# Optimization experiments

Hardware: AMD Instinct MI355X
Metric: run time of the kernel (lower is better)

Reference implementation:

```python
import jax, jax.numpy as jnp
import numpy as np
from jax import lax

# dims: B batch, L seq len, D channels, N SSM state size
BATCH, L, D, N = 8, 2048, 256, 64
MIN_DELTA = 1e-6
EPS = 1e-6


def setup_inputs() -> dict:
    key = jax.random.key(0)
    k0, k1, k2, k3, k4 = jax.random.split(key, 5)
    x = jax.random.normal(k0, (BATCH, L, D), dtype=jnp.float32)
    # log_A chosen so A = softplus(log_A) is small -> discrete_A^L stays finite in fp32
    log_A = -jax.random.normal(k1, (N, N), dtype=jnp.float32) - 3.0
    Bp = jax.random.normal(k2, (D, N), dtype=jnp.float32) * 0.02
    Cp = jax.random.normal(k3, (D, N), dtype=jnp.float32) * 0.02
    log_delta = jnp.full((D,), -8.0, dtype=jnp.float32)  # dt ~ 3.4e-4 (stability)
    skip_D = jnp.ones((D,), dtype=jnp.float32)
    W_out = jax.random.normal(k4, (D, D), dtype=jnp.float32) * (1.0 / np.sqrt(D))
    b_out = jnp.zeros((D,), dtype=jnp.float32)
    return dict(x=x, log_A=log_A, Bp=Bp, Cp=Cp, log_delta=log_delta,
                skip_D=skip_D, W_out=W_out, b_out=b_out)


def reference(x, log_A, Bp, Cp, log_delta, skip_D, W_out, b_out):
    Bsz, Lx, Dx = x.shape
    # --- discretize ---
    A = jax.nn.softplus(log_A)                                  # [N,N]
    dt = jax.nn.softplus(log_delta) + MIN_DELTA                 # [D]
    dA = jax.vmap(jax.scipy.linalg.expm)(A[None] * dt[:, None, None])  # [D,N,N]
    I = jnp.eye(A.shape[0], dtype=A.dtype)
    X = jnp.linalg.solve(A + EPS * I, Bp.T)                     # [N,D] = A^{-1} B^T
    dB = jnp.einsum('dnm,dm->dn', dA - I, X.T)                  # [D,N]
    # --- kernel k[d,l] = C_d . (dA_d)^l dB_d, via sequential recurrence (same math
    # as the explicit A-power loop, carrying the vector instead of the matrix) ---
    def step(v, _):
        return jnp.einsum('dnm,dm->dn', dA, v), jnp.sum(Cp * v, axis=-1)
    _, ks = lax.scan(step, dB, None, length=Lx)                 # ks: [L,D]
    k = ks.T                                                    # [D,L]
    # --- grouped causal conv1d: y[b,d,t] = sum_tau k[d,tau] x[b,d,t-tau] ---
    w = jnp.flip(k, -1)[:, None, :]                             # [D,1,L]
    y = lax.conv_general_dilated(
        jnp.transpose(x, (0, 2, 1)), w, (1,), [(Lx - 1, 0)],
        dimension_numbers=('NCH', 'OIH', 'NCH'), feature_group_count=Dx)
    y = jnp.transpose(y, (0, 2, 1))                             # [B,L,D]
    return (y + x * skip_D) @ W_out.T + b_out
```

## Files before the change

kernel.cpp:

```cpp
#include <hip/hip_runtime.h>

#define Bz 8
#define Lz 2048
#define Dz 256
#define Nz 64
#define SP 68
#define SA 65
#define SM 132
#define SAK 40
#define KE 4
#define KP 7
#define BSP 4
#define BPB (Bz / BSP)

typedef __attribute__((ext_vector_type(8))) short bf16x8;
typedef __attribute__((ext_vector_type(4))) float f32x4;

__device__ __forceinline__ float softplusf(float x) {
  return (x > 20.f) ? x : log1pf(expf(x));
}

__device__ __forceinline__ unsigned short f2bf(float f) {
  unsigned int u = __float_as_uint(f);
  u += 0x7fffu + ((u >> 16) & 1u);
  return (unsigned short)(u >> 16);
}

__device__ __forceinline__ void pmm_acc(const float* __restrict__ LA,
                                        const float* __restrict__ LB,
                                        float* acc, int n, int q) {
  float arow[64];
#pragma unroll
  for (int mm = 0; mm < 16; ++mm) {
    const float4 a4 = *(const float4*)(LA + n * SP + mm * 4);
    arow[4 * mm + 0] = a4.x; arow[4 * mm + 1] = a4.y;
    arow[4 * mm + 2] = a4.z; arow[4 * mm + 3] = a4.w;
  }
#pragma unroll
  for (int i = 0; i < 16; ++i) acc[i] = 0.f;
#pragma unroll 8
  for (int m = 0; m < 64; ++m) {
    const float4 b0 = *(const float4*)(LB + m * SP + q * 16 + 0);
    const float4 b1 = *(const float4*)(LB + m * SP + q * 16 + 4);
    const float4 b2 = *(const float4*)(LB + m * SP + q * 16 + 8);
    const float4 b3 = *(const float4*)(LB + m * SP + q * 16 + 12);
    const float a = arow[m];
    acc[0]  = fmaf(a, b0.x, acc[0]);  acc[1]  = fmaf(a, b0.y, acc[1]);
    acc[2]  = fmaf(a, b0.z, acc[2]);  acc[3]  = fmaf(a, b0.w, acc[3]);
    acc[4]  = fmaf(a, b1.x, acc[4]);  acc[5]  = fmaf(a, b1.y, acc[5]);
    acc[6]  = fmaf(a, b1.z, acc[6]);  acc[7]  = fmaf(a, b1.w, acc[7]);
    acc[8]  = fmaf(a, b2.x, acc[8]);  acc[9]  = fmaf(a, b2.y, acc[9]);
    acc[10] = fmaf(a, b2.z, acc[10]); acc[11] = fmaf(a, b2.w, acc[11]);
    acc[12] = fmaf(a, b3.x, acc[12]); acc[13] = fmaf(a, b3.y, acc[13]);
    acc[14] = fmaf(a, b3.z, acc[14]); acc[15] = fmaf(a, b3.w, acc[15]);
  }
}

__global__ __launch_bounds__(256) void s4_xt(const float* __restrict__ x,
                                             float* __restrict__ xT,
                                             const float* __restrict__ log_A,
                                             float* __restrict__ Apow) {
  if (blockIdx.x == 0 && blockIdx.y == 0) {
    const int i = blockIdx.z * 512 + threadIdx.x;
    Apow[i] = softplusf(log_A[i]);
    Apow[i + 256] = softplusf(log_A[i + 256]);
  }
  __shared__ float tile[64][69];
  const int t0 = blockIdx.x * 64, d0 = blockIdx.y * 64, b = blockIdx.z;
  const int rr = threadIdx.x >> 4;
  const int c4 = (threadIdx.x & 15) * 4;
#pragma unroll
  for (int p = 0; p < 4; ++p) {
    const int row = p * 16 + rr;
    const float4 v = *(const float4*)(x + ((size_t)b * Lz + t0 + row) * Dz + d0 + c4);
    tile[row][c4 + 0] = v.x; tile[row][c4 + 1] = v.y;
    tile[row][c4 + 2] = v.z; tile[row][c4 + 3] = v.w;
  }
  __syncthreads();
#pragma unroll
  for (int p = 0; p < 4; ++p) {
    const int dd = p * 16 + rr;
    float4 o;
    o.x = tile[c4 + 0][dd]; o.y = tile[c4 + 1][dd];
    o.z = tile[c4 + 2][dd]; o.w = tile[c4 + 3][dd];
    *(float4*)(xT + ((size_t)(d0 + dd) * Bz + b) * Lz + t0 + c4) = o;
  }
}

__global__ __launch_bounds__(256, 1) void s4_buildpow(
    float* __restrict__ Apow, const float* __restrict__ Bp,
    const float* __restrict__ Cp, const float* __restrict__ log_delta,
    float* __restrict__ Gk, float* __restrict__ Qk,
    float* __restrict__ kloc, float* __restrict__ dts) {
  __shared__ float As[Nz * SA];
  __shared__ float Pst[KP + 1][Nz];
  __shared__ float Qst[KE + 1][Nz];
  __shared__ float Pv[Nz], Qv[Nz], dBs[Nz];
  __shared__ float prA[4][Nz + 8], prB[4][Nz + 8];
  __shared__ float zp[KE + 1][17], zs[KE + 1];
  __shared__ alignas(16) float PA[Nz * SP];
  __shared__ alignas(16) float PB[Nz * SP];
  const int tid = threadIdx.x;
  const int d = blockIdx.x;
  const int n = tid & 63, qq = tid >> 6;

  if (d >= Dz) {
    const int role = d - Dz;
#pragma unroll
    for (int i = 0; i < 4; ++i) {
      const int e = (tid + 256 * i) * 4;
      const int r = e >> 6, c = e & 63;
      const float4 v = *(const float4*)(Apow + e);
      *(float4*)&PA[r * SP + c] = v;
      *(float4*)&PB[r * SP + c] = v;
    }
    __syncthreads();
    float acc[16];
    pmm_acc(PA, PB, acc, n, qq);
    if (role == 0) {
      float* O = Apow + (size_t)1 * 4096;
#pragma unroll
      for (int v = 0; v < 4; ++v) {
        float4 o;
        o.x = acc[4 * v]; o.y = acc[4 * v + 1];
        o.z = acc[4 * v + 2]; o.w = acc[4 * v + 3];
        *(float4*)(O + n * 64 + qq * 16 + 4 * v) = o;
      }
      return;
    }
    __syncthreads();
#pragma unroll
    for (int i = 0; i < 16; ++i) {
      PB[n * SP + qq * 16 + i] = acc[i];
      if (role == 2) PA[n * SP + qq * 16 + i] = acc[i];
    }
    __syncthreads();
    pmm_acc(PA, PB, acc, n, qq);
    float* O = Apow + (size_t)(role + 1) * 4096;
#pragma unroll
    for (int v = 0; v < 4; ++v) {
      float4 o;
      o.x = acc[4 * v]; o.y = acc[4 * v + 1];
      o.z = acc[4 * v + 2]; o.w = acc[4 * v + 3];
      *(float4*)(O + n * 64 + qq * 16 + 4 * v) = o;
    }
    return;
  }

  const float dt = softplusf(log_delta[d]) + 1e-6f;
#pragma unroll
  for (int i = 0; i < 4; ++i) {
    const int e = (tid + 256 * i) * 4;
    const int r = e >> 6, c = e & 63;
    const float4 v = *(const float4*)(Apow + e);
    As[r * SA + c] = v.x; As[r * SA + c + 1] = v.y;
    As[r * SA + c + 2] = v.z; As[r * SA + c + 3] = v.w;
  }
  if (tid < 64) {
    const float bv = Bp[d * Nz + tid], cv = Cp[d * Nz + tid];
    Pv[tid] = bv; Pst[0][tid] = bv;
    Qv[tid] = cv; Qst[0][tid] = cv;
  }
  __syncthreads();
#pragma unroll 1
  for (int k = 1; k <= KP; ++k) {
    float pp = 0.f, pq = 0.f;
#pragma unroll
    for (int mm = 0; mm < 16; ++mm) {
      const int m = qq * 16 + mm;
      pp += As[n * SA + m] * Pv[m];
      pq += As[m * SA + n] * Qv[m];
    }
    prA[qq][n] = pp; prB[qq][n] = pq;
    __syncthreads();
    if (tid < 64) {
      const float np = prA[0][tid] + prA[1][tid] + prA[2][tid] + prA[3][tid];
      Pv[tid] = np; Pst[k][tid] = np;
      if (k <= KE) {
        const float nq = prB[0][tid] + prB[1][tid] + prB[2][tid] + prB[3][tid];
        Qv[tid] = nq; Qst[k][tid] = nq;
      }
    }
    __syncthreads();
  }
  const float dtc0 = dt;
  const float dtc1 = dt * dt * 0.5f;
  const float dtc2 = dtc1 * dt * (1.f / 3.f);
  const float dtc3 = dtc2 * dt * 0.25f;
  if (tid < 64) {
    dBs[tid] = dtc0 * Pst[0][tid] + dtc1 * Pst[1][tid] +
               dtc2 * Pst[2][tid] + dtc3 * Pst[3][tid];
#pragma unroll
    for (int k = 0; k <= KE; ++k) {
      Gk[(size_t)d * ((KE + 1) * 64) + k * 64 + tid] =
          dtc0 * Pst[k][tid] + dtc1 * Pst[k + 1][tid] +
          dtc2 * Pst[k + 2][tid] + dtc3 * Pst[k + 3][tid];
      Qk[(size_t)d * ((KE + 1) * 64) + k * 64 + tid] = Qst[k][tid];
    }
  }
  __syncthreads();
  if (tid < (KE + 1) * 16) {
    const int k = tid >> 4, seg = tid & 15;
    float s = 0.f;
#pragma unroll
    for (int i = 0; i < 4; ++i) s += Qst[k][seg * 4 + i] * dBs[seg * 4 + i];
    zp[k][seg] = s;
  }
  __syncthreads();
  if (tid <= KE) {
    float s = 0.f;
#pragma unroll
    for (int seg = 0; seg < 16; ++seg) s += zp[tid][seg];
    zs[tid] = s;
  }
  __syncthreads();
  if (tid < 64) {
    const float rdt = (float)tid * dt;
    float c = 1.f, acc = zs[0];
#pragma unroll
    for (int k = 1; k <= KE; ++k) { c *= rdt / (float)k; acc += c * zs[k]; }
    kloc[d * 64 + tid] = acc;
  }
  if (tid == 0) dts[d] = dt;
}

__global__ __launch_bounds__(256) void s4_scan4(
    const float* __restrict__ xT, const float* __restrict__ Apow,
    const float* __restrict__ Gk, const float* __restrict__ dts,
    float* __restrict__ S) {
  __shared__ float Es[Nz * SA];
  __shared__ float Gs[(KE + 1) * Nz];
  __shared__ float CTs[KE + 1][66];
  __shared__ alignas(16) float Xs[BPB][64];
  __shared__ alignas(16) float Ss[BPB][64];
  __shared__ float pr[4][BPB][64];
  const int d = blockIdx.x;
  const int z = blockIdx.y;
  const int tid = threadIdx.x, n = tid & 63, q = tid >> 6;
  const int rb = tid >> 6;
  const float dt = dts[d];
  if (tid < 65) {
    const float rdt = (float)tid * dt;
    float c = 1.f;
    CTs[0][tid] = 1.f;
#pragma unroll
    for (int k = 1; k <= KE; ++k) { c *= rdt / (float)k; CTs[k][tid] = c; }
  }
  for (int idx = tid; idx < (KE + 1) * 64; idx += 256)
    Gs[idx] = Gk[(size_t)d * ((KE + 1) * 64) + idx];
  {
    float ea[16];
#pragma unroll
    for (int i = 0; i < 16; ++i) ea[i] = 0.f;
    const float dt64 = 64.f * dt;
    float ce = 1.f;
#pragma unroll 1
    for (int k = 1; k <= KE; ++k) {
      ce *= dt64 / (float)k;
      const float* Ak = Apow + (size_t)(k - 1) * 4096;
#pragma unroll
      for (int i = 0; i < 16; ++i)
        ea[i] = fmaf(ce, Ak[tid + 256 * i], ea[i]);
    }
#pragma unroll
    for (int i = 0; i < 16; ++i) {
      const int e = tid + 256 * i;
      const int r = e >> 6, c = e & 63;
      Es[r * SA + c] = ea[i] + ((r == c) ? 1.f : 0.f);
    }
  }
  __syncthreads();
  float Er[16], Ur[16];
#pragma unroll
  for (int i = 0; i < 16; ++i) Er[i] = Es[n * SA + q * 16 + i];
#pragma unroll
  for (int i = 0; i < 16; ++i) {
    const int j = q * 16 + i;
    float u = 0.f;
#pragma unroll
    for (int k = 0; k <= KE; ++k) u = fmaf(CTs[k][63 - j], Gs[k * 64 + n], u);
    Ur[i] = u;
  }
  if (rb < BPB) Ss[rb][n] = 0.f;
  const float* xd = xT + ((size_t)d * Bz + z * BPB) * Lz;
  float* Sd = S + (size_t)d * (32 * 8 * 64) + (size_t)(z * BPB) * 64;
#pragma unroll 1
  for (int c = 0; c < 32; ++c) {
    if (rb < BPB) {
      Xs[rb][n] = xd[(size_t)rb * Lz + c * 64 + n];
      Sd[c * 512 + rb * 64 + n] = Ss[rb][n];
    }
    __syncthreads();
    float acc[BPB];
#pragma unroll
    for (int b = 0; b < BPB; ++b) {
      const float4 s0 = *(const float4*)&Ss[b][q * 16 + 0];
      const float4 s1 = *(const float4*)&Ss[b][q * 16 + 4];
      const float4 s2 = *(const float4*)&Ss[b][q * 16 + 8];
      const float4 s3 = *(const float4*)&Ss[b][q * 16 + 12];
      const float4 x0 = *(const float4*)&Xs[b][q * 16 + 0];
      const float4 x1 = *(const float4*)&Xs[b][q * 16 + 4];
      const float4 x2 = *(const float4*)&Xs[b][q * 16 + 8];
      const float4 x3 = *(const float4*)&Xs[b][q * 16 + 12];
      float a = 0.f;
      a = fmaf(Er[0], s0.x, a);  a = fmaf(Er[1], s0.y, a);
      a = fmaf(Er[2], s0.z, a);  a = fmaf(Er[3], s0.w, a);
      a = fmaf(Er[4], s1.x, a);  a = fmaf(Er[5], s1.y, a);
      a = fmaf(Er[6], s1.z, a);  a = fmaf(Er[7], s1.w, a);
      a = fmaf(Er[8], s2.x, a);  a = fmaf(Er[9], s2.y, a);
      a = fmaf(Er[10], s2.z, a); a = fmaf(Er[11], s2.w, a);
      a = fmaf(Er[12], s3.x, a); a = fmaf(Er[13], s3.y, a);
      a = fmaf(Er[14], s3.z, a); a = fmaf(Er[15], s3.w, a);
      a = fmaf(Ur[0], x0.x, a);  a = fmaf(Ur[1], x0.y, a);
      a = fmaf(Ur[2], x0.z, a);  a = fmaf(Ur[3], x0.w, a);
      a = fmaf(Ur[4], x1.x, a);  a = fmaf(Ur[5], x1.y, a);
      a = fmaf(Ur[6], x1.z, a);  a = fmaf(Ur[7], x1.w, a);
      a = fmaf(Ur[8], x2.x, a);  a = fmaf(Ur[9], x2.y, a);
      a = fmaf(Ur[10], x2.z, a); a = fmaf(Ur[11], x2.w, a);
      a = fmaf(Ur[12], x3.x, a); a = fmaf(Ur[13], x3.y, a);
      a = fmaf(Ur[14], x3.z, a); a = fmaf(Ur[15], x3.w, a);
      acc[b] = a;
    }
#pragma unroll
    for (int b = 0; b < BPB; ++b) pr[q][b][n] = acc[b];
    __syncthreads();
    if (rb < BPB)
      Ss[rb][n] = pr[0][rb][n] + pr[1][rb][n] + pr[2][rb][n] + pr[3][rb][n];
    __syncthreads();
  }
}

__global__ __launch_bounds__(256, 2) void s4_out6(
    const float* __restrict__ xT, const float* __restrict__ S,
    const float* __restrict__ Qk, const float* __restrict__ kloc,
    const float* __restrict__ dts, const float* __restrict__ skip_D,
    unsigned short* __restrict__ yb) {
  __shared__ alignas(16) float Ms[64 * SM];
  __shared__ alignas(16) float Zs[64 * SM];
  __shared__ float Qs[(KE + 1) * Nz];
  __shared__ float CT[KE + 1][66];
  __shared__ float kx[64];
  const int d = blockIdx.x;
  const int ch = blockIdx.y;
  const int tid = threadIdx.x;
  const int tc = tid & 15, tr = tid >> 4;
  const float dt = dts[d];
  const float sd = skip_D[d];
  if (tid < 65) {
    const float rdt = (float)tid * dt;
    float c = 1.f;
    CT[0][tid] = 1.f;
#pragma unroll
    for (int k = 1; k <= KE; ++k) { c *= rdt / (float)k; CT[k][tid] = c; }
  }
  for (int idx = tid; idx < (KE + 1) * 64; idx += 256)
    Qs[idx] = Qk[(size_t)d * ((KE + 1) * 64) + idx];
  if (tid < 64) kx[tid] = kloc[d * 64 + tid];
  __syncthreads();
#pragma unroll
  for (int i = 0; i < 16; ++i) {
    const int e = tid + 256 * i;
    const int r = e >> 6, m = e & 63;
    float w = 0.f;
#pragma unroll
    for (int k = 0; k <= KE; ++k) w = fmaf(CT[k][r + 1], Qs[k * 64 + m], w);
    Ms[r * SM + m] = w;
  }
#pragma unroll
  for (int i = 0; i < 16; ++i) {
    const int e = tid + 256 * i;
    const int r = e >> 6, j = e & 63;
    Ms[r * SM + 64 + j] = (j <= r) ? kx[r - j] : 0.f;
  }
  const float* xd = xT + (size_t)d * Bz * Lz;
  const float* Sd = S + (size_t)d * (32 * 8 * 64);
  const int lcol = tid >> 2, seg = tid & 3;
  const int sbb = lcol & 7, sccl = lcol >> 3;
  {
    const int cc = ch * 8 + sccl;
    const float* sp = Sd + cc * 512 + sbb * 64 + seg * 16;
    const float* xp = xd + (size_t)sbb * Lz + cc * 64 + seg * 16;
    float* zrow = Zs + lcol * SM;
#pragma unroll
    for (int i = 0; i < 4; ++i) {
      *(float4*)(zrow + seg * 16 + i * 4) = *(const float4*)(sp + i * 4);
      *(float4*)(zrow + 64 + seg * 16 + i * 4) = *(const float4*)(xp + i * 4);
    }
  }
  __syncthreads();
  float acc[16];
#pragma unroll
  for (int i = 0; i < 16; ++i) acc[i] = 0.f;
#pragma unroll 4
  for (int k = 0; k < 128; k += 4) {
    float4 mv[4], zv[4];
#pragma unroll
    for (int i = 0; i < 4; ++i)
      mv[i] = *(const float4*)&Ms[(tr * 4 + i) * SM + k];
#pragma unroll
    for (int jj = 0; jj < 4; ++jj)
      zv[jj] = *(const float4*)&Zs[(tc + 16 * jj) * SM + k];
#pragma unroll
    for (int i = 0; i < 4; ++i)
#pragma unroll
      for (int jj = 0; jj < 4; ++jj) {
        acc[i * 4 + jj] = fmaf(mv[i].x, zv[jj].x, acc[i * 4 + jj]);
        acc[i * 4 + jj] = fmaf(mv[i].y, zv[jj].y, acc[i * 4 + jj]);
        acc[i * 4 + jj] = fmaf(mv[i].z, zv[jj].z, acc[i * 4 + jj]);
        acc[i * 4 + jj] = fmaf(mv[i].w, zv[jj].w, acc[i * 4 + jj]);
      }
  }
#pragma unroll
  for (int i = 0; i < 4; ++i)
#pragma unroll
    for (int jj = 0; jj < 4; ++jj)
      acc[i * 4 + jj] =
          fmaf(sd, Zs[(tc + 16 * jj) * SM + 64 + tr * 4 + i], acc[i * 4 + jj]);
  __syncthreads();
#pragma unroll
  for (int i = 0; i < 4; ++i)
#pragma unroll
    for (int jj = 0; jj < 4; ++jj)
      Zs[(tc + 16 * jj) * SM + tr * 4 + i] = acc[i * 4 + jj];
  __syncthreads();
  {
    const int cc = ch * 8 + sccl;
    unsigned short* yp =
        yb + ((size_t)d * Bz + sbb) * Lz + cc * 64 + seg * 16;
    const float* zrow = Zs + lcol * SM;
#pragma unroll
    for (int i = 0; i < 4; ++i) {
      ushort4 o;
      o.x = f2bf(zrow[seg * 16 + i * 4 + 0]);
      o.y = f2bf(zrow[seg * 16 + i * 4 + 1]);
      o.z = f2bf(zrow[seg * 16 + i * 4 + 2]);
      o.w = f2bf(zrow[seg * 16 + i * 4 + 3]);
      *(ushort4*)(yp + i * 4) = o;
    }
  }
}

__global__ __launch_bounds__(256, 2) void s4_gemm4(
    const unsigned short* __restrict__ yb, const float* __restrict__ Wo,
    const float* __restrict__ bo, float* __restrict__ out) {
  __shared__ alignas(16) unsigned short LA[128 * SAK];
  __shared__ alignas(16) unsigned short LB[64 * SAK];
  const int tid = threadIdx.x;
  const int wave = tid >> 6, lane = tid & 63;
  const int quad = lane >> 4, lq = lane & 15;
  const int r0 = blockIdx.x * 128;
  const int c0 = blockIdx.y * 64;
  const int brow = r0 >> 11, t0 = r0 & 2047;
  const int ad = tid & 31;
  const int atp = tid >> 5;
  const int bc = tid >> 2;
  const int bko = tid & 3;
  f32x4 acc[2][4];
#pragma unroll
  for (int mi = 0; mi < 2; ++mi)
#pragma unroll
    for (int ni = 0; ni < 4; ++ni)
#pragma unroll
      for (int i = 0; i < 4; ++i) acc[mi][ni][i] = 0.f;
#pragma unroll 1
  for (int ks = 0; ks < 8; ++ks) {
    const int k0 = ks * 32;
    {
      const unsigned short* src =
          yb + ((size_t)(k0 + ad) * Bz + brow) * Lz + t0 + atp * 16;
#pragma unroll
      for (int h = 0; h < 2; ++h) {
        const bf16x8 v = *(const bf16x8*)(src + h * 8);
#pragma unroll
        for (int j = 0; j < 8; ++j)
          LA[(atp * 16 + h * 8 + j) * SAK + ad] = (unsigned short)v[j];
      }
    }
    {
      const float* wsrc = Wo + (size_t)(c0 + bc) * Dz + k0 + bko * 8;
      const float4 w0 = *(const float4*)(wsrc);
      const float4 w1 = *(const float4*)(wsrc + 4);
      bf16x8 wv;
      wv[0] = (short)f2bf(w0.x); wv[1] = (short)f2bf(w0.y);
      wv[2] = (short)f2bf(w0.z); wv[3] = (short)f2bf(w0.w);
      wv[4] = (short)f2bf(w1.x); wv[5] = (short)f2bf(w1.y);
      wv[6] = (short)f2bf(w1.z); wv[7] = (short)f2bf(w1.w);
      *(bf16x8*)&LB[bc * SAK + bko * 8] = wv;
    }
    __syncthreads();
    bf16x8 af[2], bfr[4];
#pragma unroll
    for (int mi = 0; mi < 2; ++mi)
      af[mi] = *(const bf16x8*)&LA[(wave * 32 + mi * 16 + lq) * SAK + quad * 8];
#pragma unroll
    for (int ni = 0; ni < 4; ++ni)
      bfr[ni] = *(const bf16x8*)&LB[(ni * 16 + lq) * SAK + quad * 8];
#pragma unroll
    for (int mi = 0; mi < 2; ++mi)
#pragma unroll
      for (int ni = 0; ni < 4; ++ni)
        acc[mi][ni] = __builtin_amdgcn_mfma_f32_16x16x32_bf16(
            af[mi], bfr[ni], acc[mi][ni], 0, 0, 0);
    __syncthreads();
  }
  float bb[4];
#pragma unroll
  for (int ni = 0; ni < 4; ++ni) bb[ni] = bo[c0 + ni * 16 + lq];
#pragma unroll
  for (int mi = 0; mi < 2; ++mi)
#pragma unroll
    for (int i = 0; i < 4; ++i) {
      const int row = r0 + wave * 32 + mi * 16 + quad * 4 + i;
#pragma unroll
      for (int ni = 0; ni < 4; ++ni)
        out[(size_t)row * Dz + c0 + ni * 16 + lq] = acc[mi][ni][i] + bb[ni];
    }
}

extern "C" void kernel_launch(void* const* d_in, const int* in_sizes, int n_in,
                              void* d_out, int out_size, void* d_ws, size_t ws_size,
                              hipStream_t stream) {
  const float* x         = (const float*)d_in[0];
  const float* log_A     = (const float*)d_in[1];
  const float* Bp        = (const float*)d_in[2];
  const float* Cp        = (const float*)d_in[3];
  const float* log_delta = (const float*)d_in[4];
  const float* skip_D    = (const float*)d_in[5];
  const float* W_out     = (const float*)d_in[6];
  const float* b_out     = (const float*)d_in[7];
  float* out = (float*)d_out;

  float* xT   = (float*)d_ws;
  float* ybf  = xT + (size_t)Dz * Bz * Lz;
  float* S    = ybf + (size_t)Dz * Bz * Lz;
  float* Apow = S + (size_t)Dz * (32 * 8 * 64);
  float* Gk   = Apow + (size_t)8 * 4096;
  float* Qk   = Gk + (size_t)Dz * (KE + 1) * 64;
  float* kloc = Qk + (size_t)Dz * (KE + 1) * 64;
  float* dts  = kloc + (size_t)Dz * 64;
  unsigned short* yb = (unsigned short*)ybf;

  hipLaunchKernelGGL(s4_xt, dim3(Lz / 64, Dz / 64, Bz), dim3(256), 0, stream,
                     x, xT, log_A, Apow);
  hipLaunchKernelGGL(s4_buildpow, dim3(Dz + 3), dim3(256), 0, stream,
                     Apow, Bp, Cp, log_delta, Gk, Qk, kloc, dts);
  hipLaunchKernelGGL(s4_scan4, dim3(Dz, BSP), dim3(256), 0, stream,
                     xT, Apow, Gk, dts, S);
  hipLaunchKernelGGL(s4_out6, dim3(Dz, 4), dim3(256), 0, stream,
                     xT, S, Qk, kloc, dts, skip_D, yb);
  hipLaunchKernelGGL(s4_gemm4, dim3((Bz * Lz) / 128, Dz / 64), dim3(256), 0, stream,
                     yb, W_out, b_out, out);
}
```

Before: 168.2 us.

## Convert output-chunk GEMM in s4_out to bf16 MFMA with folded skip term

Rewrites the per-channel output kernel so the 64x128 by 128x64 product runs on bf16 MFMA 16x16x32 instructions instead of scalar fp32 FMAs. Operands are converted to bf16 when staged into shared memory, which halves LDS footprint and allows more blocks per CU. The skip connection is folded into the local kernel diagonal, and results are written straight from accumulators without a shared-memory transpose. This trades precision, since state, inputs and kernel weights are now rounded to bf16, for much higher matrix throughput.

```diff
diff --git a/kernel.cpp b/kernel.cpp
--- a/kernel.cpp
+++ b/kernel.cpp
@@ -6,8 +6,8 @@
 #define Nz 64
 #define SP 68
 #define SA 65
-#define SM 132
 #define SAK 40
+#define SKB 136
 #define KE 4
 #define KP 7
 #define BSP 4
@@ -330,22 +330,22 @@
   }
 }
 
-__global__ __launch_bounds__(256, 2) void s4_out6(
+__global__ __launch_bounds__(256, 4) void s4_out7(
     const float* __restrict__ xT, const float* __restrict__ S,
     const float* __restrict__ Qk, const float* __restrict__ kloc,
     const float* __restrict__ dts, const float* __restrict__ skip_D,
     unsigned short* __restrict__ yb) {
-  __shared__ alignas(16) float Ms[64 * SM];
-  __shared__ alignas(16) float Zs[64 * SM];
+  __shared__ alignas(16) unsigned short Msb[64 * SKB];
+  __shared__ alignas(16) unsigned short Zsb[64 * SKB];
   __shared__ float Qs[(KE + 1) * Nz];
   __shared__ float CT[KE + 1][66];
-  __shared__ float kx[64];
+  __shared__ unsigned short kxb[64];
   const int d = blockIdx.x;
   const int ch = blockIdx.y;
   const int tid = threadIdx.x;
-  const int tc = tid & 15, tr = tid >> 4;
+  const int wave = tid >> 6, lane = tid & 63;
+  const int quad = lane >> 4, lq = lane & 15;
   const float dt = dts[d];
-  const float sd = skip_D[d];
   if (tid < 65) {
     const float rdt = (float)tid * dt;
     float c = 1.f;
@@ -355,8 +355,29 @@
   }
   for (int idx = tid; idx < (KE + 1) * 64; idx += 256)
     Qs[idx] = Qk[(size_t)d * ((KE + 1) * 64) + idx];
-  if (tid < 64) kx[tid] = kloc[d * 64 + tid];
-  __syncthreads();
+  if (tid < 64)
+    kxb[tid] = f2bf(kloc[d * 64 + tid] + ((tid == 0) ? skip_D[d] : 0.f));
+
+  const float* xd = xT + (size_t)d * Bz * Lz;
+  const float* Sd = S + (size_t)d * (32 * 8 * 64);
+#pragma unroll
+  for (int p = 0; p < 8; ++p) {
+    const int u = tid + 256 * p;
+    const int col = u >> 5;
+    const int sub = u & 31;
+    const int k0 = sub * 4;
+    const int bb = col & 7, ccl = col >> 3;
+    const int cc = ch * 8 + ccl;
+    const float* src = (k0 < 64)
+        ? (Sd + cc * 512 + bb * 64 + k0)
+        : (xd + (size_t)bb * Lz + cc * 64 + (k0 - 64));
+    const float4 v = *(const float4*)src;
+    ushort4 o;
+    o.x = f2bf(v.x); o.y = f2bf(v.y); o.z = f2bf(v.z); o.w = f2bf(v.w);
+    *(ushort4*)&Zsb[col * SKB + k0] = o;
+  }
+  __syncthreads();
+
 #pragma unroll
   for (int i = 0; i < 16; ++i) {
     const int e = tid + 256 * i;
@@ -364,79 +385,41 @@
     float w = 0.f;
 #pragma unroll
     for (int k = 0; k <= KE; ++k) w = fmaf(CT[k][r + 1], Qs[k * 64 + m], w);
-    Ms[r * SM + m] = w;
+    Msb[r * SKB + m] = f2bf(w);
   }
 #pragma unroll
   for (int i = 0; i < 16; ++i) {
     const int e = tid + 256 * i;
     const int r = e >> 6, j = e & 63;
-    Ms[r * SM + 64 + j] = (j <= r) ? kx[r - j] : 0.f;
-  }
-  const float* xd = xT + (size_t)d * Bz * Lz;
-  const float* Sd = S + (size_t)d * (32 * 8 * 64);
-  const int lcol = tid >> 2, seg = tid & 3;
-  const int sbb = lcol & 7, sccl = lcol >> 3;
-  {
-    const int cc = ch * 8 + sccl;
-    const float* sp = Sd + cc * 512 + sbb * 64 + seg * 16;
-    const float* xp = xd + (size_t)sbb * Lz + cc * 64 + seg * 16;
-    float* zrow = Zs + lcol * SM;
-#pragma unroll
-    for (int i = 0; i < 4; ++i) {
-      *(float4*)(zrow + seg * 16 + i * 4) = *(const float4*)(sp + i * 4);
-      *(float4*)(zrow + 64 + seg * 16 + i * 4) = *(const float4*)(xp + i * 4);
-    }
-  }
-  __syncthreads();
-  float acc[16];
-#pragma unroll
-  for (int i = 0; i < 16; ++i) acc[i] = 0.f;
-#pragma unroll 4
-  for (int k = 0; k < 128; k += 4) {
-    float4 mv[4], zv[4];
-#pragma unroll
-    for (int i = 0; i < 4; ++i)
-      mv[i] = *(const float4*)&Ms[(tr * 4 + i) * SM + k];
-#pragma unroll
-    for (int jj = 0; jj < 4; ++jj)
-      zv[jj] = *(const float4*)&Zs[(tc + 16 * jj) * SM + k];
-#pragma unroll
-    for (int i = 0; i < 4; ++i)
-#pragma unroll
-      for (int jj = 0; jj < 4; ++jj) {
-        acc[i * 4 + jj] = fmaf(mv[i].x, zv[jj].x, acc[i * 4 + jj]);
-        acc[i * 4 + jj] = fmaf(mv[i].y, zv[jj].y, acc[i * 4 + jj]);
-        acc[i * 4 + jj] = fmaf(mv[i].z, zv[jj].z, acc[i * 4 + jj]);
-        acc[i * 4 + jj] = fmaf(mv[i].w, zv[jj].w, acc[i * 4 + jj]);
-      }
-  }
-#pragma unroll
-  for (int i = 0; i < 4; ++i)
-#pragma unroll
-    for (int jj = 0; jj < 4; ++jj)
-      acc[i * 4 + jj] =
-          fmaf(sd, Zs[(tc + 16 * jj) * SM + 64 + tr * 4 + i], acc[i * 4 + jj]);
-  __syncthreads();
-#pragma unroll
-  for (int i = 0; i < 4; ++i)
-#pragma unroll
-    for (int jj = 0; jj < 4; ++jj)
-      Zs[(tc + 16 * jj) * SM + tr * 4 + i] = acc[i * 4 + jj];
-  __syncthreads();
-  {
-    const int cc = ch * 8 + sccl;
-    unsigned short* yp =
-        yb + ((size_t)d * Bz + sbb) * Lz + cc * 64 + seg * 16;
-    const float* zrow = Zs + lcol * SM;
-#pragma unroll
-    for (int i = 0; i < 4; ++i) {
-      ushort4 o;
-      o.x = f2bf(zrow[seg * 16 + i * 4 + 0]);
-      o.y = f2bf(zrow[seg * 16 + i * 4 + 1]);
-      o.z = f2bf(zrow[seg * 16 + i * 4 + 2]);
-      o.w = f2bf(zrow[seg * 16 + i * 4 + 3]);
-      *(ushort4*)(yp + i * 4) = o;
-    }
+    Msb[r * SKB + 64 + j] = (j <= r) ? kxb[r - j] : (unsigned short)0;
+  }
+  __syncthreads();
+
+  f32x4 acc[4];
+#pragma unroll
+  for (int ni = 0; ni < 4; ++ni)
+#pragma unroll
+    for (int i = 0; i < 4; ++i) acc[ni][i] = 0.f;
+#pragma unroll
+  for (int ks = 0; ks < 4; ++ks) {
+    const bf16x8 af =
+        *(const bf16x8*)&Msb[(wave * 16 + lq) * SKB + ks * 32 + quad * 8];
+#pragma unroll
+    for (int ni = 0; ni < 4; ++ni) {
+      const bf16x8 bfr =
+          *(const bf16x8*)&Zsb[(ni * 16 + lq) * SKB + ks * 32 + quad * 8];
+      acc[ni] = __builtin_amdgcn_mfma_f32_16x16x32_bf16(af, bfr, acc[ni], 0, 0, 0);
+    }
+  }
+#pragma unroll
+  for (int ni = 0; ni < 4; ++ni) {
+    const int col = ni * 16 + lq;
+    const int bb = col & 7, ccl = col >> 3;
+    const int cc = ch * 8 + ccl;
+    ushort4 o;
+    o.x = f2bf(acc[ni][0]); o.y = f2bf(acc[ni][1]);
+    o.z = f2bf(acc[ni][2]); o.w = f2bf(acc[ni][3]);
+    *(ushort4*)(yb + ((size_t)d * Bz + bb) * Lz + cc * 64 + wave * 16 + quad * 4) = o;
   }
 }
 
@@ -546,7 +529,7 @@
                      Apow, Bp, Cp, log_delta, Gk, Qk, kloc, dts);
   hipLaunchKernelGGL(s4_scan4, dim3(Dz, BSP), dim3(256), 0, stream,
                      xT, Apow, Gk, dts, S);
-  hipLaunchKernelGGL(s4_out6, dim3(Dz, 4), dim3(256), 0, stream,
+  hipLaunchKernelGGL(s4_out7, dim3(Dz, 4), dim3(256), 0, stream,
                      xT, S, Qk, kloc, dts, skip_D, yb);
   hipLaunchKernelGGL(s4_gemm4, dim3((Bz * Lz) / 128, Dz / 64), dim3(256), 0, stream,
                      yb, W_out, b_out, out);
```

New measurement: 154.1 us. 1.09x faster.
